# Optimization experiments

Measured on AMD Instinct MI355X. Metric: run time of the kernel, lower is better.

Reference implementation:

```python
import jax, jax.numpy as jnp
import numpy as np

N_OSC = 32
CONV = 1000.0  # convergence_factor


def _cpg_ode(y, ia, ifr, cw, pb):
    # Faithful to CPGOde.forward, including its unpacking order:
    # (amplitudes, amplitudes_dot, phases) = (y[:n], y[n:2n], y[2n:3n])
    n = N_OSC
    a = y[:n]
    a_dot = y[n:2 * n]
    ph = y[2 * n:3 * n]
    phase_dots = ifr + jnp.sum(a[:, None] * cw * jnp.sin(ph[None, :] - ph[:, None] - pb), axis=1)
    a_dd = CONV * (CONV / 4.0 * (ia - a) - a_dot)
    # states_to_tensor(amplitudes_dot, phase_dots, amplitudes_dot_dot)
    return jnp.concatenate([a_dot, phase_dots, a_dd])


def _rk4_38_step(f, y, h):
    # torchdiffeq 'rk4' = rk4_alt_step_func (3/8 rule), one step over t=[0, h]
    k1 = f(y)
    k2 = f(y + h * k1 / 3.0)
    k3 = f(y + h * (k2 - k1 / 3.0))
    k4 = f(y + h * (k1 - k2 + k3))
    return y + h * 0.125 * (k1 + 3.0 * (k2 + k3) + k4)


def _mlp(x, Ws, bs):
    # Linear stack with ReLU between layers, none after the last
    for i, (W, b) in enumerate(zip(Ws, bs)):
        x = W @ x + b
        if i < len(Ws) - 1:
            x = jax.nn.relu(x)
    return x


def _init_linear(key, fan_in, fan_out):
    kW, kb = jax.random.split(key)
    bound = 1.0 / np.sqrt(fan_in)
    W = jax.random.uniform(kW, (fan_out, fan_in), minval=-bound, maxval=bound, dtype=jnp.float32)
    b = jax.random.uniform(kb, (fan_out,), minval=-bound, maxval=bound, dtype=jnp.float32)
    return W, b


def setup_inputs() -> dict:
    key = jax.random.key(0)
    ks = jax.random.split(key, 10)
    n = N_OSC
    n_params = 2 * n + 2 * n * n  # 2112
    in_dims = [2049, 4096, 4096, n_params]  # input_layers[0]+1, ..., final param layer
    out_dims = [2 * n, 2048, 2048, 1024]
    inp = {}
    inp["state"] = jax.random.normal(ks[0], (3 * n,), dtype=jnp.float32) * 0.1
    inp["x"] = jax.random.normal(ks[1], (2048,), dtype=jnp.float32)
    inp["timestep"] = jnp.array(0.01, dtype=jnp.float32)
    for i in range(3):
        W, b = _init_linear(ks[2 + i], in_dims[i], in_dims[i + 1])
        inp[f"in_W{i}"] = W
        inp[f"in_b{i}"] = b
    for i in range(3):
        W, b = _init_linear(ks[5 + i], out_dims[i], out_dims[i + 1])
        inp[f"out_W{i}"] = W
        inp[f"out_b{i}"] = b
    return inp


def reference(state, x, timestep,
              in_W0, in_b0, in_W1, in_b1, in_W2, in_b2,
              out_W0, out_b0, out_W1, out_b1, out_W2, out_b2):
    n = N_OSC
    # append timestep scalar to the input features
    x = jnp.concatenate([x, timestep[None]])
    params = _mlp(x, [in_W0, in_W1, in_W2], [in_b0, in_b1, in_b2])
    ia = params[:n]
    ifr = params[n:2 * n]
    cw = params[2 * n:2 * n + n * n].reshape(n, n)
    pb = params[2 * n + n * n:].reshape(n, n)
    f = lambda y: _cpg_ode(y, ia, ifr, cw, pb)
    new_state = _rk4_38_step(f, state, timestep)
    a = new_state[:n]
    ph = new_state[n:2 * n]
    cpg_out = jnp.concatenate([a * jnp.cos(ph), a * jnp.sin(ph)])
    out = _mlp(cpg_out, [out_W0, out_W1, out_W2], [out_b0, out_b1, out_b2])
    return (jax.lax.stop_gradient(new_state), out)
```

## Files before the change

kernel.cpp:

```cpp
#include <hip/hip_runtime.h>
#include <stdint.h>

template<int RELU, int TSCOL>
__global__ __launch_bounds__(256) void gemv_k(
    const float* __restrict__ W, const float* __restrict__ B,
    const float* __restrict__ x, const float* __restrict__ ts,
    float* __restrict__ y, int rows, int cols)
{
    int wv   = threadIdx.x >> 6;
    int lane = threadIdx.x & 63;
    int row  = blockIdx.x * 4 + wv;
    if (row >= rows) return;

    int n = TSCOL ? cols - 1 : cols;
    const float* w = W + (size_t)row * (size_t)cols;

    int mis = (int)(((uintptr_t)w >> 2) & 3);
    int start = (4 - mis) & 3;
    if (start > n) start = n;

    float sum = 0.0f;
    if (lane < start) sum += w[lane] * x[lane];

    int nv = (n - start) >> 2;
    const float4* wp = (const float4*)(w + start);
    const float* xs = x + start;

    int g = lane;
    for (; g + 448 < nv; g += 512) {
        float4 u0 = wp[g];
        float4 u1 = wp[g + 64];
        float4 u2 = wp[g + 128];
        float4 u3 = wp[g + 192];
        float4 u4 = wp[g + 256];
        float4 u5 = wp[g + 320];
        float4 u6 = wp[g + 384];
        float4 u7 = wp[g + 448];
        const float* x0 = xs + 4 * g;
        sum += u0.x * x0[0]    + u0.y * x0[1]    + u0.z * x0[2]    + u0.w * x0[3];
        sum += u1.x * x0[256]  + u1.y * x0[257]  + u1.z * x0[258]  + u1.w * x0[259];
        sum += u2.x * x0[512]  + u2.y * x0[513]  + u2.z * x0[514]  + u2.w * x0[515];
        sum += u3.x * x0[768]  + u3.y * x0[769]  + u3.z * x0[770]  + u3.w * x0[771];
        sum += u4.x * x0[1024] + u4.y * x0[1025] + u4.z * x0[1026] + u4.w * x0[1027];
        sum += u5.x * x0[1280] + u5.y * x0[1281] + u5.z * x0[1282] + u5.w * x0[1283];
        sum += u6.x * x0[1536] + u6.y * x0[1537] + u6.z * x0[1538] + u6.w * x0[1539];
        sum += u7.x * x0[1792] + u7.y * x0[1793] + u7.z * x0[1794] + u7.w * x0[1795];
    }
    for (; g < nv; g += 64) {
        float4 u = wp[g];
        const float* xp = xs + 4 * g;
        sum += u.x * xp[0] + u.y * xp[1] + u.z * xp[2] + u.w * xp[3];
    }
    int t = start + nv * 4 + lane;
    if (t < n) sum += w[t] * x[t];
    if (TSCOL && lane == 0) sum += w[n] * ts[0];

    #pragma unroll
    for (int off = 32; off > 0; off >>= 1) sum += __shfl_down(sum, off);

    if (lane == 0) {
        float r = sum + B[row];
        if (RELU) r = fmaxf(r, 0.0f);
        y[row] = r;
    }
}

__global__ __launch_bounds__(64) void ode_k(
    const float* __restrict__ state, const float* __restrict__ ts,
    const float* __restrict__ params, float* __restrict__ cpg,
    float* __restrict__ out_state)
{
    const float CONV = 1000.0f;
    __shared__ float s_cw[32 * 33];
    __shared__ float s_spb[32 * 33];
    __shared__ float s_cpb[32 * 33];
    __shared__ float s_s[32], s_c[32];
    int tid = threadIdx.x;

    for (int k = tid; k < 1024; k += 64) {
        int p = k + (k >> 5);
        s_cw[p] = params[64 + k];
        float sp, cp;
        sincosf(params[1088 + k], &sp, &cp);
        s_spb[p] = sp;
        s_cpb[p] = cp;
    }
    __syncthreads();

    bool act = (tid < 32);
    int i = tid;
    float ia = 0.f, ifr = 0.f, y0a = 0.f, y0b = 0.f, y0c = 0.f;
    if (act) {
        ia  = params[i];
        ifr = params[32 + i];
        y0a = state[i];
        y0b = state[32 + i];
        y0c = state[64 + i];
    }
    float h = ts[0];

    float k1a=0,k1b=0,k1c=0, k2a=0,k2b=0,k2c=0, k3a=0,k3b=0,k3c=0, k4a=0,k4b=0,k4c=0;

    auto do_eval = [&](float a, float ad, float ph,
                       float& fa, float& fb, float& fc) {
        __syncthreads();
        if (act) {
            float s, c;
            sincosf(ph, &s, &c);
            s_s[i] = s; s_c[i] = c;
        }
        __syncthreads();
        if (act) {
            float si = s_s[i], ci = s_c[i];
            float ssum = 0.0f;
            #pragma unroll
            for (int j = 0; j < 32; j++) {
                float sj = s_s[j], cj = s_c[j];
                float sdp = sj * ci - cj * si;
                float cdp = cj * ci + sj * si;
                int p = i * 33 + j;
                float sv = sdp * s_cpb[p] - cdp * s_spb[p];
                ssum += s_cw[p] * sv;
            }
            fa = ad;
            fb = ifr + a * ssum;
            fc = CONV * (CONV * 0.25f * (ia - a) - ad);
        }
    };

    do_eval(y0a, y0b, y0c, k1a, k1b, k1c);
    do_eval(y0a + h * k1a / 3.0f,
            y0b + h * k1b / 3.0f,
            y0c + h * k1c / 3.0f, k2a, k2b, k2c);
    do_eval(y0a + h * (k2a - k1a / 3.0f),
            y0b + h * (k2b - k1b / 3.0f),
            y0c + h * (k2c - k1c / 3.0f), k3a, k3b, k3c);
    do_eval(y0a + h * (k1a - k2a + k3a),
            y0b + h * (k1b - k2b + k3b),
            y0c + h * (k1c - k2c + k3c), k4a, k4b, k4c);

    if (act) {
        float na = y0a + h * 0.125f * (k1a + 3.0f * (k2a + k3a) + k4a);
        float nb = y0b + h * 0.125f * (k1b + 3.0f * (k2b + k3b) + k4b);
        float nc = y0c + h * 0.125f * (k1c + 3.0f * (k2c + k3c) + k4c);
        out_state[i]      = na;
        out_state[32 + i] = nb;
        out_state[64 + i] = nc;
        cpg[i]      = na * cosf(nb);
        cpg[32 + i] = na * sinf(nb);
    }
}

extern "C" void kernel_launch(void* const* d_in, const int* in_sizes, int n_in,
                              void* d_out, int out_size, void* d_ws, size_t ws_size,
                              hipStream_t stream) {
    const float* state = (const float*)d_in[0];
    const float* x     = (const float*)d_in[1];
    const float* ts    = (const float*)d_in[2];
    const float* inW0  = (const float*)d_in[3];
    const float* inb0  = (const float*)d_in[4];
    const float* inW1  = (const float*)d_in[5];
    const float* inb1  = (const float*)d_in[6];
    const float* inW2  = (const float*)d_in[7];
    const float* inb2  = (const float*)d_in[8];
    const float* oW0   = (const float*)d_in[9];
    const float* ob0   = (const float*)d_in[10];
    const float* oW1   = (const float*)d_in[11];
    const float* ob1   = (const float*)d_in[12];
    const float* oW2   = (const float*)d_in[13];
    const float* ob2   = (const float*)d_in[14];

    float* ws  = (float*)d_ws;
    float* h0  = ws;
    float* h1  = ws + 4096;
    float* pr  = ws + 8192;
    float* cpg = ws + 10304;
    float* g0  = ws + 10368;
    float* g1  = ws + 12416;

    float* out = (float*)d_out;

    gemv_k<1,1><<<1024, 256, 0, stream>>>(inW0, inb0, x,   ts,      h0, 4096, 2049);
    gemv_k<1,0><<<1024, 256, 0, stream>>>(inW1, inb1, h0,  nullptr, h1, 4096, 4096);
    gemv_k<0,0><<< 528, 256, 0, stream>>>(inW2, inb2, h1,  nullptr, pr, 2112, 4096);
    ode_k<<<1, 64, 0, stream>>>(state, ts, pr, cpg, out);
    gemv_k<1,0><<< 512, 256, 0, stream>>>(oW0,  ob0,  cpg, nullptr, g0, 2048, 64);
    gemv_k<1,0><<< 512, 256, 0, stream>>>(oW1,  ob1,  g0,  nullptr, g1, 2048, 2048);
    gemv_k<0,0><<< 256, 256, 0, stream>>>(oW2,  ob2,  g1,  nullptr, out + 96, 1024, 2048);
}
```

Baseline: 220.4 us.

## Fuse ODE step into first output GEMV and vectorize x loads

```diff
diff --git a/kernel.cpp b/kernel.cpp
--- a/kernel.cpp
+++ b/kernel.cpp
@@ -1,7 +1,7 @@
 #include <hip/hip_runtime.h>
 #include <stdint.h>
 
-template<int RELU, int TSCOL>
+template<int RELU, int TSCOL, int XVEC>
 __global__ __launch_bounds__(256) void gemv_k(
     const float* __restrict__ W, const float* __restrict__ B,
     const float* __restrict__ x, const float* __restrict__ ts,
@@ -14,45 +14,74 @@
 
     int n = TSCOL ? cols - 1 : cols;
     const float* w = W + (size_t)row * (size_t)cols;
-
-    int mis = (int)(((uintptr_t)w >> 2) & 3);
-    int start = (4 - mis) & 3;
-    if (start > n) start = n;
-
     float sum = 0.0f;
-    if (lane < start) sum += w[lane] * x[lane];
-
-    int nv = (n - start) >> 2;
-    const float4* wp = (const float4*)(w + start);
-    const float* xs = x + start;
-
-    int g = lane;
-    for (; g + 448 < nv; g += 512) {
-        float4 u0 = wp[g];
-        float4 u1 = wp[g + 64];
-        float4 u2 = wp[g + 128];
-        float4 u3 = wp[g + 192];
-        float4 u4 = wp[g + 256];
-        float4 u5 = wp[g + 320];
-        float4 u6 = wp[g + 384];
-        float4 u7 = wp[g + 448];
-        const float* x0 = xs + 4 * g;
-        sum += u0.x * x0[0]    + u0.y * x0[1]    + u0.z * x0[2]    + u0.w * x0[3];
-        sum += u1.x * x0[256]  + u1.y * x0[257]  + u1.z * x0[258]  + u1.w * x0[259];
-        sum += u2.x * x0[512]  + u2.y * x0[513]  + u2.z * x0[514]  + u2.w * x0[515];
-        sum += u3.x * x0[768]  + u3.y * x0[769]  + u3.z * x0[770]  + u3.w * x0[771];
-        sum += u4.x * x0[1024] + u4.y * x0[1025] + u4.z * x0[1026] + u4.w * x0[1027];
-        sum += u5.x * x0[1280] + u5.y * x0[1281] + u5.z * x0[1282] + u5.w * x0[1283];
-        sum += u6.x * x0[1536] + u6.y * x0[1537] + u6.z * x0[1538] + u6.w * x0[1539];
-        sum += u7.x * x0[1792] + u7.y * x0[1793] + u7.z * x0[1794] + u7.w * x0[1795];
-    }
-    for (; g < nv; g += 64) {
-        float4 u = wp[g];
-        const float* xp = xs + 4 * g;
-        sum += u.x * xp[0] + u.y * xp[1] + u.z * xp[2] + u.w * xp[3];
-    }
-    int t = start + nv * 4 + lane;
-    if (t < n) sum += w[t] * x[t];
+
+    if (XVEC) {
+        int nv = n >> 2;
+        const float4* wp = (const float4*)w;
+        const float4* xp = (const float4*)x;
+        int g = lane;
+        for (; g + 448 < nv; g += 512) {
+            float4 u0 = wp[g];       float4 v0 = xp[g];
+            float4 u1 = wp[g + 64];  float4 v1 = xp[g + 64];
+            float4 u2 = wp[g + 128]; float4 v2 = xp[g + 128];
+            float4 u3 = wp[g + 192]; float4 v3 = xp[g + 192];
+            float4 u4 = wp[g + 256]; float4 v4 = xp[g + 256];
+            float4 u5 = wp[g + 320]; float4 v5 = xp[g + 320];
+            float4 u6 = wp[g + 384]; float4 v6 = xp[g + 384];
+            float4 u7 = wp[g + 448]; float4 v7 = xp[g + 448];
+            sum += u0.x*v0.x + u0.y*v0.y + u0.z*v0.z + u0.w*v0.w;
+            sum += u1.x*v1.x + u1.y*v1.y + u1.z*v1.z + u1.w*v1.w;
+            sum += u2.x*v2.x + u2.y*v2.y + u2.z*v2.z + u2.w*v2.w;
+            sum += u3.x*v3.x + u3.y*v3.y + u3.z*v3.z + u3.w*v3.w;
+            sum += u4.x*v4.x + u4.y*v4.y + u4.z*v4.z + u4.w*v4.w;
+            sum += u5.x*v5.x + u5.y*v5.y + u5.z*v5.z + u5.w*v5.w;
+            sum += u6.x*v6.x + u6.y*v6.y + u6.z*v6.z + u6.w*v6.w;
+            sum += u7.x*v7.x + u7.y*v7.y + u7.z*v7.z + u7.w*v7.w;
+        }
+        for (; g < nv; g += 64) {
+            float4 u = wp[g];
+            float4 v = xp[g];
+            sum += u.x*v.x + u.y*v.y + u.z*v.z + u.w*v.w;
+        }
+        int t = nv * 4 + lane;
+        if (t < n) sum += w[t] * x[t];
+    } else {
+        int mis = (int)(((uintptr_t)w >> 2) & 3);
+        int start = (4 - mis) & 3;
+        if (start > n) start = n;
+        if (lane < start) sum += w[lane] * x[lane];
+        int nv = (n - start) >> 2;
+        const float4* wp = (const float4*)(w + start);
+        const float* xs = x + start;
+        int g = lane;
+        for (; g + 448 < nv; g += 512) {
+            float4 u0 = wp[g];
+            float4 u1 = wp[g + 64];
+            float4 u2 = wp[g + 128];
+            float4 u3 = wp[g + 192];
+            float4 u4 = wp[g + 256];
+            float4 u5 = wp[g + 320];
+            float4 u6 = wp[g + 384];
+            float4 u7 = wp[g + 448];
+            const float* x0 = xs + 4 * g;
+            sum += u0.x * x0[0]    + u0.y * x0[1]    + u0.z * x0[2]    + u0.w * x0[3];
+            sum += u1.x * x0[256]  + u1.y * x0[257]  + u1.z * x0[258]  + u1.w * x0[259];
+            sum += u2.x * x0[512]  + u2.y * x0[513]  + u2.z * x0[514]  + u2.w * x0[515];
+            sum += u3.x * x0[768]  + u3.y * x0[769]  + u3.z * x0[770]  + u3.w * x0[771];
+            sum += u4.x * x0[1024] + u4.y * x0[1025] + u4.z * x0[1026] + u4.w * x0[1027];
+            sum += u5.x * x0[1280] + u5.y * x0[1281] + u5.z * x0[1282] + u5.w * x0[1283];
+            sum += u6.x * x0[1536] + u6.y * x0[1537] + u6.z * x0[1538] + u6.w * x0[1539];
+            sum += u7.x * x0[1792] + u7.y * x0[1793] + u7.z * x0[1794] + u7.w * x0[1795];
+        }
+        for (; g < nv; g += 64) {
+            float4 u = wp[g];
+            const float* xp = xs + 4 * g;
+            sum += u.x * xp[0] + u.y * xp[1] + u.z * xp[2] + u.w * xp[3];
+        }
+        int t = start + nv * 4 + lane;
+        if (t < n) sum += w[t] * x[t];
+    }
     if (TSCOL && lane == 0) sum += w[n] * ts[0];
 
     #pragma unroll
@@ -65,19 +94,21 @@
     }
 }
 
-__global__ __launch_bounds__(64) void ode_k(
+__global__ __launch_bounds__(256) void ode_ow0_k(
     const float* __restrict__ state, const float* __restrict__ ts,
-    const float* __restrict__ params, float* __restrict__ cpg,
-    float* __restrict__ out_state)
+    const float* __restrict__ params,
+    const float* __restrict__ oW0, const float* __restrict__ ob0,
+    float* __restrict__ g0, float* __restrict__ out_state)
 {
     const float CONV = 1000.0f;
     __shared__ float s_cw[32 * 33];
     __shared__ float s_spb[32 * 33];
     __shared__ float s_cpb[32 * 33];
     __shared__ float s_s[32], s_c[32];
+    __shared__ float s_cpg[64];
     int tid = threadIdx.x;
 
-    for (int k = tid; k < 1024; k += 64) {
+    for (int k = tid; k < 1024; k += 256) {
         int p = k + (k >> 5);
         s_cw[p] = params[64 + k];
         float sp, cp;
@@ -143,12 +174,23 @@
         float na = y0a + h * 0.125f * (k1a + 3.0f * (k2a + k3a) + k4a);
         float nb = y0b + h * 0.125f * (k1b + 3.0f * (k2b + k3b) + k4b);
         float nc = y0c + h * 0.125f * (k1c + 3.0f * (k2c + k3c) + k4c);
-        out_state[i]      = na;
-        out_state[32 + i] = nb;
-        out_state[64 + i] = nc;
-        cpg[i]      = na * cosf(nb);
-        cpg[32 + i] = na * sinf(nb);
-    }
+        if (blockIdx.x == 0) {
+            out_state[i]      = na;
+            out_state[32 + i] = nb;
+            out_state[64 + i] = nc;
+        }
+        s_cpg[i]      = na * cosf(nb);
+        s_cpg[32 + i] = na * sinf(nb);
+    }
+    __syncthreads();
+
+    int wv   = tid >> 6;
+    int lane = tid & 63;
+    int row  = blockIdx.x * 4 + wv;
+    float sum = oW0[(size_t)row * 64 + lane] * s_cpg[lane];
+    #pragma unroll
+    for (int off = 32; off > 0; off >>= 1) sum += __shfl_down(sum, off);
+    if (lane == 0) g0[row] = fmaxf(sum + ob0[row], 0.0f);
 }
 
 extern "C" void kernel_launch(void* const* d_in, const int* in_sizes, int n_in,
@@ -174,17 +216,15 @@
     float* h0  = ws;
     float* h1  = ws + 4096;
     float* pr  = ws + 8192;
-    float* cpg = ws + 10304;
     float* g0  = ws + 10368;
     float* g1  = ws + 12416;
 
     float* out = (float*)d_out;
 
-    gemv_k<1,1><<<1024, 256, 0, stream>>>(inW0, inb0, x,   ts,      h0, 4096, 2049);
-    gemv_k<1,0><<<1024, 256, 0, stream>>>(inW1, inb1, h0,  nullptr, h1, 4096, 4096);
-    gemv_k<0,0><<< 528, 256, 0, stream>>>(inW2, inb2, h1,  nullptr, pr, 2112, 4096);
-    ode_k<<<1, 64, 0, stream>>>(state, ts, pr, cpg, out);
-    gemv_k<1,0><<< 512, 256, 0, stream>>>(oW0,  ob0,  cpg, nullptr, g0, 2048, 64);
-    gemv_k<1,0><<< 512, 256, 0, stream>>>(oW1,  ob1,  g0,  nullptr, g1, 2048, 2048);
-    gemv_k<0,0><<< 256, 256, 0, stream>>>(oW2,  ob2,  g1,  nullptr, out + 96, 1024, 2048);
+    gemv_k<1,1,0><<<1024, 256, 0, stream>>>(inW0, inb0, x,   ts,      h0, 4096, 2049);
+    gemv_k<1,0,1><<<1024, 256, 0, stream>>>(inW1, inb1, h0,  nullptr, h1, 4096, 4096);
+    gemv_k<0,0,1><<< 528, 256, 0, stream>>>(inW2, inb2, h1,  nullptr, pr, 2112, 4096);
+    ode_ow0_k<<<512, 256, 0, stream>>>(state, ts, pr, oW0, ob0, g0, out);
+    gemv_k<1,0,1><<< 512, 256, 0, stream>>>(oW1,  ob1,  g0,  nullptr, g1, 2048, 2048);
+    gemv_k<0,0,1><<< 256, 256, 0, stream>>>(oW2,  ob2,  g1,  nullptr, out + 96, 1024, 2048);
 }
```

Result: no change. 217.4 us (-1.3%).
